# Performance work log

Hardware: AMD Instinct MI355X
Metric: run time of the kernel (lower is better)

## Reference

```python
import jax, jax.numpy as jnp
import numpy as np

# ---- static config (mirrors init_kwargs) ----
PILLAR_SIZE = 0.075
X_MIN, Y_MIN, Z_MIN = -54.0, -54.0, -5.0
X_MAX, Y_MAX, Z_MAX = 54.0, 54.0, 3.0
GRID_W = int(round((X_MAX - X_MIN) / PILLAR_SIZE))  # 1440
GRID_H = int(round((Y_MAX - Y_MIN) / PILLAR_SIZE))  # 1440
B = 4            # batch (lidar frames)
N = 800_000      # total points across batch
M = 120_000      # total occupied pillars across batch
C_IN = 5         # raw point features (x,y,z,intensity,timestamp)
C_GRP = 6 + C_IN # (xyz - pillar_center, xyz, pt_feature)
C_MLP = 32       # shared MLP output width
BN_EPS = 1e-3


def _pillar_centers(pillar_indices):
    """pillar_indices: (M,3) int [b, y, x] -> (M,3) float centers."""
    pi = pillar_indices.astype(jnp.float32)
    cx = (pi[:, 2] + 0.5) * PILLAR_SIZE + X_MIN
    cy = (pi[:, 1] + 0.5) * PILLAR_SIZE + Y_MIN
    cz = jnp.full_like(cx, 0.5 * (Z_MIN + Z_MAX))
    return jnp.stack([cx, cy, cz], axis=1)


def setup_inputs() -> dict:
    key = jax.random.key(0)
    ks = jax.random.split(key, 8)
    # occupied pillar cells [b, y, x]
    pil_b = jax.random.randint(ks[0], (M,), 0, B, dtype=jnp.int32)
    pil_y = jax.random.randint(ks[1], (M,), 0, GRID_H, dtype=jnp.int32)
    pil_x = jax.random.randint(ks[2], (M,), 0, GRID_W, dtype=jnp.int32)
    pillar_indices = jnp.stack([pil_b, pil_y, pil_x], axis=1)
    # each point belongs to exactly one pillar
    pillar_set_indices = jax.random.randint(ks[3], (N,), 0, M, dtype=jnp.int32)
    centers = _pillar_centers(pillar_indices)
    noise = jax.random.normal(ks[4], (N, 3), dtype=jnp.float32)
    noise = noise * jnp.array([0.3 * PILLAR_SIZE, 0.3 * PILLAR_SIZE, 1.5], jnp.float32)
    xyz = centers[pillar_set_indices] + noise  # points near their pillar center
    pt_feature = jax.random.normal(ks[5], (N, C_IN), dtype=jnp.float32)
    # shared MLP params: Linear(no bias) + BatchNorm1d(gamma, beta)
    W1 = jax.random.normal(ks[6], (C_GRP, C_MLP), dtype=jnp.float32) * np.float32(1.0 / np.sqrt(C_GRP))
    gamma1 = jnp.ones((C_MLP,), jnp.float32)
    beta1 = jnp.zeros((C_MLP,), jnp.float32)
    xyz_batch_cnt = jnp.full((B,), N // B, jnp.int32)
    return dict(xyz=xyz, pt_feature=pt_feature, W1=W1, gamma1=gamma1, beta1=beta1,
                pillar_indices=pillar_indices, pillar_set_indices=pillar_set_indices,
                xyz_batch_cnt=xyz_batch_cnt)


def reference(xyz, pt_feature, W1, gamma1, beta1, pillar_indices, pillar_set_indices, xyz_batch_cnt):
    # --- PillarQueryAndGroup: gather per-point grouped features ---
    centers = _pillar_centers(pillar_indices)            # (M, 3)
    ctr = centers[pillar_set_indices]                    # (N, 3) gather
    group_features = jnp.concatenate([xyz - ctr, xyz, pt_feature], axis=1)  # (N, 6+C)
    # --- shared MLP: Linear(no bias) -> BatchNorm1d (train-mode stats) -> ReLU ---
    h = group_features @ W1                              # (N, C_MLP)
    mean = jnp.mean(h, axis=0)
    var = jnp.var(h, axis=0)                             # biased, as torch BN uses for normalization
    h = (h - mean) * jax.lax.rsqrt(var + BN_EPS) * gamma1 + beta1
    h = jax.nn.relu(h)
    # --- scatter-max pool over pillars (CUDA scatter_max inits to 0) ---
    pooled = jax.ops.segment_max(h, pillar_set_indices, num_segments=M)
    pillar_features = jnp.maximum(pooled, 0.0)           # empty pillars -> 0; h >= 0 after ReLU
    return pillar_features                               # (M, C_MLP); dense features of SparseConvTensor
```

## Files before the change

kernel.cpp:

```cpp
#include <hip/hip_runtime.h>


#define CMLP 32
#define BN_EPS 1e-3f
#define PSIZE 0.075f
#define XMIN -54.0f
#define YMIN -54.0f
#define CZ   -1.0f
#define NREP 64
#define SCATB 4096

__device__ __forceinline__ unsigned enc_f(float x) {
  unsigned b = __float_as_uint(x);
  return (b & 0x80000000u) ? ~b : (b | 0x80000000u);
}
__device__ __forceinline__ float dec_f(unsigned u) {
  unsigned b = (u & 0x80000000u) ? (u & 0x7fffffffu) : ~u;
  return __uint_as_float(b);
}

__global__ void __launch_bounds__(256) scatter_stats_kernel(
    const float* __restrict__ xyz, const float* __restrict__ ptf,
    const float* __restrict__ W1, const float* __restrict__ gamma,
    const int* __restrict__ pil, const int* __restrict__ sidx,
    float* __restrict__ stats_rep, unsigned* __restrict__ outenc, int N) {
  const int tid = threadIdx.x;
  const int c = tid & 31;
  const float w0 = W1[0 * CMLP + c], w1 = W1[1 * CMLP + c];
  const float w2 = W1[2 * CMLP + c];
  const float wx = w0 + W1[3 * CMLP + c];
  const float wy = w1 + W1[4 * CMLP + c];
  const float wz = w2 + W1[5 * CMLP + c];
  const float nw0 = -w0, nw1 = -w1;
  const float c0 = -CZ * w2;
  const float w6 = W1[6 * CMLP + c], w7 = W1[7 * CMLP + c];
  const float w8 = W1[8 * CMLP + c], w9 = W1[9 * CMLP + c];
  const float w10 = W1[10 * CMLP + c];
  const float sgn = (gamma[c] < 0.f) ? -1.f : 1.f;
  float s = 0.f, ss = 0.f;
  const int hw0 = (blockIdx.x * 256 + tid) >> 5;
  const int nhw = (SCATB * 256) >> 5;
  int p = hw0;
  int m = (p < N) ? __builtin_nontemporal_load(&sidx[p]) : 0;
  while (p < N) {
    const int pn = p + nhw;
    const int mn = (pn < N) ? __builtin_nontemporal_load(&sidx[pn]) : 0;
    float cx = fmaf((float)pil[3 * m + 2] + 0.5f, PSIZE, XMIN);
    float cy = fmaf((float)pil[3 * m + 1] + 0.5f, PSIZE, YMIN);
    float x = __builtin_nontemporal_load(&xyz[3 * p]);
    float y = __builtin_nontemporal_load(&xyz[3 * p + 1]);
    float z = __builtin_nontemporal_load(&xyz[3 * p + 2]);
    float h = c0;
    h = fmaf(x, wx, h);
    h = fmaf(y, wy, h);
    h = fmaf(z, wz, h);
    h = fmaf(cx, nw0, h);
    h = fmaf(cy, nw1, h);
    h = fmaf(__builtin_nontemporal_load(&ptf[5 * p + 0]), w6, h);
    h = fmaf(__builtin_nontemporal_load(&ptf[5 * p + 1]), w7, h);
    h = fmaf(__builtin_nontemporal_load(&ptf[5 * p + 2]), w8, h);
    h = fmaf(__builtin_nontemporal_load(&ptf[5 * p + 3]), w9, h);
    h = fmaf(__builtin_nontemporal_load(&ptf[5 * p + 4]), w10, h);
    s += h;
    ss = fmaf(h, h, ss);
    atomicMax(&outenc[m * CMLP + c], enc_f(sgn * h));
    p = pn;
    m = mn;
  }
  s += __shfl_xor(s, 32);
  ss += __shfl_xor(ss, 32);
  __shared__ float red[4][64];
  const int wave = tid >> 6, lane = tid & 63;
  if (lane < 32) {
    red[wave][lane] = s;
    red[wave][32 + lane] = ss;
  }
  __syncthreads();
  if (tid < 64) {
    float v = red[0][tid] + red[1][tid] + red[2][tid] + red[3][tid];
    atomicAdd(&stats_rep[(blockIdx.x & (NREP - 1)) * 64 + tid], v);
  }
}

__global__ void finalize_kernel(const float* __restrict__ gamma,
                                const float* __restrict__ beta,
                                const float* __restrict__ stats_rep,
                                float* __restrict__ affine, float invN) {
  int c = threadIdx.x;
  if (c < CMLP) {
    float s = 0.f, ss = 0.f;
    for (int r = 0; r < NREP; r++) {
      s += stats_rep[r * 64 + c];
      ss += stats_rep[r * 64 + 32 + c];
    }
    float mean = s * invN;
    float var = ss * invN - mean * mean;
    float sc = gamma[c] * rsqrtf(var + BN_EPS);
    affine[c] = sc;
    affine[CMLP + c] = beta[c] - mean * sc;
  }
}

__global__ void __launch_bounds__(256) transform_kernel(
    unsigned* __restrict__ io, const float* __restrict__ affine, int total) {
  int i = blockIdx.x * 256 + threadIdx.x;
  if (i < total) {
    unsigned u = io[i];
    int c = i & 31;
    float v = 0.f;
    if (u) v = fmaxf(fmaf(fabsf(affine[c]), dec_f(u), affine[CMLP + c]), 0.f);
    io[i] = __float_as_uint(v);
  }
}

extern "C" void kernel_launch(void* const* d_in, const int* in_sizes, int n_in,
                              void* d_out, int out_size, void* d_ws, size_t ws_size,
                              hipStream_t stream) {
  const float* xyz = (const float*)d_in[0];
  const float* ptf = (const float*)d_in[1];
  const float* W1 = (const float*)d_in[2];
  const float* gamma = (const float*)d_in[3];
  const float* beta = (const float*)d_in[4];
  const int* pil = (const int*)d_in[5];
  const int* sidx = (const int*)d_in[6];
  unsigned* out = (unsigned*)d_out;

  int N = in_sizes[0] / 3;

  float* stats_rep = (float*)d_ws;
  float* affine = (float*)((char*)d_ws + NREP * 64 * sizeof(float));

  hipMemsetAsync(stats_rep, 0, NREP * 64 * sizeof(float), stream);
  hipMemsetAsync(out, 0, (size_t)out_size * sizeof(unsigned), stream);

  scatter_stats_kernel<<<SCATB, 256, 0, stream>>>(xyz, ptf, W1, gamma, pil,
                                                  sidx, stats_rep, out, N);
  finalize_kernel<<<1, 64, 0, stream>>>(gamma, beta, stats_rep, affine,
                                        1.0f / (float)N);
  transform_kernel<<<(out_size + 255) / 256, 256, 0, stream>>>(out, affine,
                                                               out_size);
}
```

Baseline: 189.3 us.

## Partition scatter atomics by pillar index across XCD-aligned block groups

The scatter kernel now gives each group of 8 consecutive blocks a contiguous chunk of points. Each block in the group handles only the points whose pillar index mod 8 equals blockIdx mod 8. Because blocks are dispatched round-robin across the 8 XCDs, all atomicMax traffic for a given pillar should stay on one XCD's L2, and each XCD's slice of the output may fit in its cache. The cost is that every point's pillar index is read eight times, and each half-wave loops serially over a ballot mask of owned points, which adds control overhead and can load-balance unevenly.

Measured after the change: 177.2 us. 6.3% less time.

```diff
diff --git a/kernel.cpp b/kernel.cpp
--- a/kernel.cpp
+++ b/kernel.cpp
@@ -23,49 +23,69 @@
     const float* __restrict__ xyz, const float* __restrict__ ptf,
     const float* __restrict__ W1, const float* __restrict__ gamma,
     const int* __restrict__ pil, const int* __restrict__ sidx,
-    float* __restrict__ stats_rep, unsigned* __restrict__ outenc, int N) {
+    float* __restrict__ stats_rep, unsigned* __restrict__ outenc,
+    int N, int chunk) {
   const int tid = threadIdx.x;
   const int c = tid & 31;
+  const int half = tid & 32;
+  const int q = blockIdx.x & 7;
+  const int sid = ((blockIdx.x >> 3) << 3) + (tid >> 5);
+  const int base = sid * chunk;
   const float w0 = W1[0 * CMLP + c], w1 = W1[1 * CMLP + c];
   const float w2 = W1[2 * CMLP + c];
   const float wx = w0 + W1[3 * CMLP + c];
   const float wy = w1 + W1[4 * CMLP + c];
   const float wz = w2 + W1[5 * CMLP + c];
   const float nw0 = -w0, nw1 = -w1;
-  const float c0 = -CZ * w2;
+  const float cc0 = -CZ * w2;
   const float w6 = W1[6 * CMLP + c], w7 = W1[7 * CMLP + c];
   const float w8 = W1[8 * CMLP + c], w9 = W1[9 * CMLP + c];
   const float w10 = W1[10 * CMLP + c];
   const float sgn = (gamma[c] < 0.f) ? -1.f : 1.f;
   float s = 0.f, ss = 0.f;
-  const int hw0 = (blockIdx.x * 256 + tid) >> 5;
-  const int nhw = (SCATB * 256) >> 5;
-  int p = hw0;
-  int m = (p < N) ? __builtin_nontemporal_load(&sidx[p]) : 0;
-  while (p < N) {
-    const int pn = p + nhw;
-    const int mn = (pn < N) ? __builtin_nontemporal_load(&sidx[pn]) : 0;
-    float cx = fmaf((float)pil[3 * m + 2] + 0.5f, PSIZE, XMIN);
-    float cy = fmaf((float)pil[3 * m + 1] + 0.5f, PSIZE, YMIN);
-    float x = __builtin_nontemporal_load(&xyz[3 * p]);
-    float y = __builtin_nontemporal_load(&xyz[3 * p + 1]);
-    float z = __builtin_nontemporal_load(&xyz[3 * p + 2]);
-    float h = c0;
-    h = fmaf(x, wx, h);
-    h = fmaf(y, wy, h);
-    h = fmaf(z, wz, h);
-    h = fmaf(cx, nw0, h);
-    h = fmaf(cy, nw1, h);
-    h = fmaf(__builtin_nontemporal_load(&ptf[5 * p + 0]), w6, h);
-    h = fmaf(__builtin_nontemporal_load(&ptf[5 * p + 1]), w7, h);
-    h = fmaf(__builtin_nontemporal_load(&ptf[5 * p + 2]), w8, h);
-    h = fmaf(__builtin_nontemporal_load(&ptf[5 * p + 3]), w9, h);
-    h = fmaf(__builtin_nontemporal_load(&ptf[5 * p + 4]), w10, h);
-    s += h;
-    ss = fmaf(h, h, ss);
-    atomicMax(&outenc[m * CMLP + c], enc_f(sgn * h));
-    p = pn;
-    m = mn;
+
+  int i = 0;
+  int idx = base + c;
+  int mb = (idx < N) ? sidx[idx] : 0;
+  bool vb = (c < chunk) && (idx < N);
+  while (i < chunk) {
+    const int inext = i + 32;
+    int mn = 0;
+    bool vn = false;
+    if (inext < chunk) {
+      int idxn = base + inext + c;
+      vn = (inext + c < chunk) && (idxn < N);
+      mn = (idxn < N) ? sidx[idxn] : 0;
+    }
+    const bool own = vb && ((mb & 7) == q);
+    unsigned long long bal = __ballot(own);
+    unsigned mask = (unsigned)(bal >> half);
+    while (mask) {
+      const int src = __ffs(mask) - 1;
+      mask &= mask - 1;
+      const int m = __shfl(mb, src + half);
+      const int p = base + i + src;
+      float cx = fmaf((float)pil[3 * m + 2] + 0.5f, PSIZE, XMIN);
+      float cy = fmaf((float)pil[3 * m + 1] + 0.5f, PSIZE, YMIN);
+      float x = xyz[3 * p], y = xyz[3 * p + 1], z = xyz[3 * p + 2];
+      float h = cc0;
+      h = fmaf(x, wx, h);
+      h = fmaf(y, wy, h);
+      h = fmaf(z, wz, h);
+      h = fmaf(cx, nw0, h);
+      h = fmaf(cy, nw1, h);
+      h = fmaf(ptf[5 * p + 0], w6, h);
+      h = fmaf(ptf[5 * p + 1], w7, h);
+      h = fmaf(ptf[5 * p + 2], w8, h);
+      h = fmaf(ptf[5 * p + 3], w9, h);
+      h = fmaf(ptf[5 * p + 4], w10, h);
+      s += h;
+      ss = fmaf(h, h, ss);
+      atomicMax(&outenc[m * CMLP + c], enc_f(sgn * h));
+    }
+    i = inext;
+    mb = mn;
+    vb = vn;
   }
   s += __shfl_xor(s, 32);
   ss += __shfl_xor(ss, 32);
@@ -126,6 +146,7 @@
   unsigned* out = (unsigned*)d_out;
 
   int N = in_sizes[0] / 3;
+  int chunk = (N + SCATB - 1) / SCATB;
 
   float* stats_rep = (float*)d_ws;
   float* affine = (float*)((char*)d_ws + NREP * 64 * sizeof(float));
@@ -134,7 +155,8 @@
   hipMemsetAsync(out, 0, (size_t)out_size * sizeof(unsigned), stream);
 
   scatter_stats_kernel<<<SCATB, 256, 0, stream>>>(xyz, ptf, W1, gamma, pil,
-                                                  sidx, stats_rep, out, N);
+                                                  sidx, stats_rep, out, N,
+                                                  chunk);
   finalize_kernel<<<1, 64, 0, stream>>>(gamma, beta, stats_rep, affine,
                                         1.0f / (float)N);
   transform_kernel<<<(out_size + 255) / 256, 256, 0, stream>>>(out, affine,
```
